# Optimization experiments

Hardware: AMD Instinct MI355X
Metric: run time of the kernel (lower is better)

## Reference

```python
import jax, jax.numpy as jnp
import numpy as np

UNITS = 50

def setup_inputs() -> dict:
    key = jax.random.key(0)
    ks = jax.random.split(key, 6)
    B, T, F = 4096, 128, 64
    scale = 0.1
    return {
        "x": jax.random.normal(ks[0], (B, T, F), dtype=jnp.float32),
        "W": jax.random.normal(ks[1], (F, 3 * UNITS), dtype=jnp.float32) * scale,
        "U": jax.random.normal(ks[2], (UNITS, 3 * UNITS), dtype=jnp.float32) * scale,
        "b": jax.random.normal(ks[3], (2, 3 * UNITS), dtype=jnp.float32) * scale,
        "Wd": jax.random.normal(ks[4], (UNITS, 1), dtype=jnp.float32) * scale,
        "bd": jnp.zeros((1,), dtype=jnp.float32),
    }

def reference(x, W, U, b, Wd, bd):
    # Keras GRU, reset_after=True, activation=relu, recurrent_activation=sigmoid.
    B, T, F = x.shape
    u = UNITS
    # Precompute input projections for all timesteps: [B,T,3u]
    xp = jnp.einsum('btf,fk->btk', x, W) + b[0]
    xp = jnp.moveaxis(xp, 1, 0)  # [T,B,3u]
    bi = b[1]

    def step(h, xt):
        hp = h @ U + bi                     # [B,3u]
        xz, xr, xh = xt[:, :u], xt[:, u:2*u], xt[:, 2*u:]
        hz, hr, hh = hp[:, :u], hp[:, u:2*u], hp[:, 2*u:]
        z = jax.nn.sigmoid(xz + hz)
        r = jax.nn.sigmoid(xr + hr)
        hcand = jax.nn.relu(xh + r * hh)
        h_new = z * h + (1.0 - z) * hcand
        return h_new, None

    h0 = jnp.zeros((B, u), dtype=x.dtype)
    hT, _ = jax.lax.scan(step, h0, xp)
    # Dropout is identity at inference; Dense head:
    return hT @ Wd + bd
```

## Files before the change

### kernel.cpp

```cpp
#include <hip/hip_runtime.h>
#include <math.h>

typedef _Float16 v8h __attribute__((ext_vector_type(8)));
typedef float v4f __attribute__((ext_vector_type(4)));

#define UNITS    50
#define K3       150
#define FDIM     64
#define TSTEPS   128
#define BATCH    4096
#define NB       16
#define H16S     72
#define H32S     52

#if __has_builtin(__builtin_amdgcn_exp2f)
__device__ __forceinline__ float fast_exp2(float x) { return __builtin_amdgcn_exp2f(x); }
#else
__device__ __forceinline__ float fast_exp2(float x) { return exp2f(x); }
#endif
#if __has_builtin(__builtin_amdgcn_rcpf)
__device__ __forceinline__ float fast_rcp(float x) { return __builtin_amdgcn_rcpf(x); }
#else
__device__ __forceinline__ float fast_rcp(float x) { return 1.0f / x; }
#endif

__global__ __launch_bounds__(256, 1)
void gru_4w(const float* __restrict__ x, const float* __restrict__ W,
            const float* __restrict__ U, const float* __restrict__ bv,
            const float* __restrict__ Wd, const float* __restrict__ bd,
            float* __restrict__ out) {
    __shared__ _Float16 hs16[2][NB * H16S];
    __shared__ float    hs32[NB * H32S];

    const int tid  = threadIdx.x;
    const int nt   = tid >> 6;
    const int lane = tid & 63;
    const int n    = lane & 15;
    const int quad = lane >> 4;
    const int b0   = blockIdx.x * NB;
    const int c    = nt * 16 + n;

    for (int i = tid; i < NB * H16S; i += 256) {
        _Float16 v = ((i % H16S) == 50) ? (_Float16)1.f : (_Float16)0.f;
        hs16[0][i] = v;
        hs16[1][i] = v;
    }

    v8h Bz[4], Br[4], Bh[4];
    #pragma unroll
    for (int kt = 0; kt < 4; ++kt) {
        v8h fz, fr, fh;
        #pragma unroll
        for (int j = 0; j < 8; ++j) {
            const int k = kt * 32 + quad * 8 + j;
            float vz = 0.f, vr = 0.f, vh = 0.f;
            if (c < UNITS) {
                if (k < FDIM) {
                    vz = W[k * K3 + c];
                    vr = W[k * K3 + 50 + c];
                    vh = W[k * K3 + 100 + c];
                } else if (k < FDIM + UNITS) {
                    const int ur = k - FDIM;
                    vz = U[ur * K3 + c];
                    vr = U[ur * K3 + 50 + c];
                    vh = U[ur * K3 + 100 + c];
                } else if (k == FDIM + UNITS) {
                    vh = bv[250 + c];
                }
            }
            fz[j] = (_Float16)vz; fr[j] = (_Float16)vr; fh[j] = (_Float16)vh;
        }
        Bz[kt] = fz; Br[kt] = fr; Bh[kt] = fh;
    }

    const float CE = -1.44269504f;
    float bzc = 0.f, brc = 0.f, bx = 0.f;
    if (c < UNITS) {
        bzc = CE * (bv[c]      + bv[150 + c]);
        brc = CE * (bv[50 + c] + bv[200 + c]);
        bx  = bv[100 + c];
    }

    v4f h32 = {0.f, 0.f, 0.f, 0.f};

    const float* xbase = x + ((size_t)(b0 + n) * TSTEPS) * FDIM + quad * 8;
    v4f px0 = *(const v4f*)(xbase + 0);
    v4f px1 = *(const v4f*)(xbase + 4);
    v4f px2 = *(const v4f*)(xbase + 32);
    v4f px3 = *(const v4f*)(xbase + 36);

    __syncthreads();

    for (int t = 0; t < TSTEPS; ++t) {
        const _Float16* hrd = hs16[t & 1];
        _Float16*       hwr = hs16[(t + 1) & 1];

        v8h A0, A1;
        #pragma unroll
        for (int j = 0; j < 4; ++j) {
            A0[j]     = (_Float16)px0[j];
            A0[j + 4] = (_Float16)px1[j];
            A1[j]     = (_Float16)px2[j];
            A1[j + 4] = (_Float16)px3[j];
        }
        v8h A2 = *(const v8h*)(&hrd[n * H16S + quad * 8]);
        v8h A3 = *(const v8h*)(&hrd[n * H16S + 32 + quad * 8]);

        if (t + 1 < TSTEPS) {
            const float* xp = xbase + (size_t)(t + 1) * FDIM;
            px0 = *(const v4f*)(xp + 0);
            px1 = *(const v4f*)(xp + 4);
            px2 = *(const v4f*)(xp + 32);
            px3 = *(const v4f*)(xp + 36);
        }

        const v4f zero4 = {0.f, 0.f, 0.f, 0.f};
        v4f ax = {bx, bx, bx, bx};
        v4f az = __builtin_amdgcn_mfma_f32_16x16x32_f16(A0, Bz[0], zero4, 0, 0, 0);
        az     = __builtin_amdgcn_mfma_f32_16x16x32_f16(A1, Bz[1], az,    0, 0, 0);
        v4f ar = __builtin_amdgcn_mfma_f32_16x16x32_f16(A0, Br[0], zero4, 0, 0, 0);
        ar     = __builtin_amdgcn_mfma_f32_16x16x32_f16(A1, Br[1], ar,    0, 0, 0);
        ax     = __builtin_amdgcn_mfma_f32_16x16x32_f16(A0, Bh[0], ax,    0, 0, 0);
        ax     = __builtin_amdgcn_mfma_f32_16x16x32_f16(A1, Bh[1], ax,    0, 0, 0);
        az     = __builtin_amdgcn_mfma_f32_16x16x32_f16(A2, Bz[2], az,    0, 0, 0);
        az     = __builtin_amdgcn_mfma_f32_16x16x32_f16(A3, Bz[3], az,    0, 0, 0);
        ar     = __builtin_amdgcn_mfma_f32_16x16x32_f16(A2, Br[2], ar,    0, 0, 0);
        ar     = __builtin_amdgcn_mfma_f32_16x16x32_f16(A3, Br[3], ar,    0, 0, 0);
        v4f ah = __builtin_amdgcn_mfma_f32_16x16x32_f16(A2, Bh[2], zero4, 0, 0, 0);
        ah     = __builtin_amdgcn_mfma_f32_16x16x32_f16(A3, Bh[3], ah,    0, 0, 0);

        #pragma unroll
        for (int r = 0; r < 4; ++r) {
            const float ez = fast_exp2(fmaf(az[r], CE, bzc));
            const float er = fast_exp2(fmaf(ar[r], CE, brc));
            const float pz = 1.f + ez;
            const float pr = 1.f + er;
            const float d  = fast_rcp(pz * pr);
            const float zg = d * pr;
            const float rg = d * pz;
            const float hc = fmaxf(fmaf(rg, ah[r], ax[r]), 0.f);
            const float hn = fmaf(zg, h32[r] - hc, hc);
            h32[r] = hn;
            if (c < UNITS)
                hwr[(quad * 4 + r) * H16S + c] = (_Float16)hn;
        }
        __syncthreads();
    }

    if (c < UNITS) {
        #pragma unroll
        for (int r = 0; r < 4; ++r)
            hs32[(quad * 4 + r) * H32S + c] = h32[r];
    }
    __syncthreads();
    if (tid < NB) {
        float acc = bd[0];
        #pragma unroll
        for (int u = 0; u < UNITS; ++u)
            acc = fmaf(hs32[tid * H32S + u], Wd[u], acc);
        out[b0 + tid] = acc;
    }
}

extern "C" void kernel_launch(void* const* d_in, const int* in_sizes, int n_in,
                              void* d_out, int out_size, void* d_ws, size_t ws_size,
                              hipStream_t stream) {
    const float* x    = (const float*)d_in[0];
    const float* W    = (const float*)d_in[1];
    const float* U    = (const float*)d_in[2];
    const float* bv   = (const float*)d_in[3];
    const float* Wd   = (const float*)d_in[4];
    const float* bd   = (const float*)d_in[5];
    float* out = (float*)d_out;

    dim3 grid(BATCH / NB);
    dim3 block(256);
    gru_4w<<<grid, block, 0, stream>>>(x, W, U, bv, Wd, bd, out);
}
```

Before: 272.7 us.

## Use LDS-only barrier, double-buffer x prefetch, split x/h MFMA chains

```diff
diff --git a/kernel.cpp b/kernel.cpp
--- a/kernel.cpp
+++ b/kernel.cpp
@@ -24,11 +24,16 @@
 __device__ __forceinline__ float fast_rcp(float x) { return 1.0f / x; }
 #endif
 
+__device__ __forceinline__ void sync_lds() {
+    asm volatile("s_waitcnt lgkmcnt(0)" ::: "memory");
+    __builtin_amdgcn_s_barrier();
+}
+
 __global__ __launch_bounds__(256, 1)
-void gru_4w(const float* __restrict__ x, const float* __restrict__ W,
-            const float* __restrict__ U, const float* __restrict__ bv,
-            const float* __restrict__ Wd, const float* __restrict__ bd,
-            float* __restrict__ out) {
+void gru_nodrain(const float* __restrict__ x, const float* __restrict__ W,
+                 const float* __restrict__ U, const float* __restrict__ bv,
+                 const float* __restrict__ Wd, const float* __restrict__ bd,
+                 float* __restrict__ out) {
     __shared__ _Float16 hs16[2][NB * H16S];
     __shared__ float    hs32[NB * H32S];
 
@@ -84,67 +89,76 @@
     v4f h32 = {0.f, 0.f, 0.f, 0.f};
 
     const float* xbase = x + ((size_t)(b0 + n) * TSTEPS) * FDIM + quad * 8;
-    v4f px0 = *(const v4f*)(xbase + 0);
-    v4f px1 = *(const v4f*)(xbase + 4);
-    v4f px2 = *(const v4f*)(xbase + 32);
-    v4f px3 = *(const v4f*)(xbase + 36);
+    v4f px[2][4];
+    #pragma unroll
+    for (int s = 0; s < 2; ++s) {
+        const float* xp = xbase + (size_t)s * FDIM;
+        px[s][0] = *(const v4f*)(xp + 0);
+        px[s][1] = *(const v4f*)(xp + 4);
+        px[s][2] = *(const v4f*)(xp + 32);
+        px[s][3] = *(const v4f*)(xp + 36);
+    }
 
     __syncthreads();
 
+    #pragma unroll 2
     for (int t = 0; t < TSTEPS; ++t) {
+        const int pb = t & 1;
         const _Float16* hrd = hs16[t & 1];
         _Float16*       hwr = hs16[(t + 1) & 1];
 
+        v8h A2 = *(const v8h*)(&hrd[n * H16S + quad * 8]);
+        v8h A3 = *(const v8h*)(&hrd[n * H16S + 32 + quad * 8]);
         v8h A0, A1;
         #pragma unroll
         for (int j = 0; j < 4; ++j) {
-            A0[j]     = (_Float16)px0[j];
-            A0[j + 4] = (_Float16)px1[j];
-            A1[j]     = (_Float16)px2[j];
-            A1[j + 4] = (_Float16)px3[j];
+            A0[j]     = (_Float16)px[pb][0][j];
+            A0[j + 4] = (_Float16)px[pb][1][j];
+            A1[j]     = (_Float16)px[pb][2][j];
+            A1[j + 4] = (_Float16)px[pb][3][j];
         }
-        v8h A2 = *(const v8h*)(&hrd[n * H16S + quad * 8]);
-        v8h A3 = *(const v8h*)(&hrd[n * H16S + 32 + quad * 8]);
 
-        if (t + 1 < TSTEPS) {
-            const float* xp = xbase + (size_t)(t + 1) * FDIM;
-            px0 = *(const v4f*)(xp + 0);
-            px1 = *(const v4f*)(xp + 4);
-            px2 = *(const v4f*)(xp + 32);
-            px3 = *(const v4f*)(xp + 36);
+        if (t + 2 < TSTEPS) {
+            const float* xp = xbase + (size_t)(t + 2) * FDIM;
+            px[pb][0] = *(const v4f*)(xp + 0);
+            px[pb][1] = *(const v4f*)(xp + 4);
+            px[pb][2] = *(const v4f*)(xp + 32);
+            px[pb][3] = *(const v4f*)(xp + 36);
         }
 
         const v4f zero4 = {0.f, 0.f, 0.f, 0.f};
-        v4f ax = {bx, bx, bx, bx};
-        v4f az = __builtin_amdgcn_mfma_f32_16x16x32_f16(A0, Bz[0], zero4, 0, 0, 0);
-        az     = __builtin_amdgcn_mfma_f32_16x16x32_f16(A1, Bz[1], az,    0, 0, 0);
-        v4f ar = __builtin_amdgcn_mfma_f32_16x16x32_f16(A0, Br[0], zero4, 0, 0, 0);
-        ar     = __builtin_amdgcn_mfma_f32_16x16x32_f16(A1, Br[1], ar,    0, 0, 0);
-        ax     = __builtin_amdgcn_mfma_f32_16x16x32_f16(A0, Bh[0], ax,    0, 0, 0);
-        ax     = __builtin_amdgcn_mfma_f32_16x16x32_f16(A1, Bh[1], ax,    0, 0, 0);
-        az     = __builtin_amdgcn_mfma_f32_16x16x32_f16(A2, Bz[2], az,    0, 0, 0);
-        az     = __builtin_amdgcn_mfma_f32_16x16x32_f16(A3, Bz[3], az,    0, 0, 0);
-        ar     = __builtin_amdgcn_mfma_f32_16x16x32_f16(A2, Br[2], ar,    0, 0, 0);
-        ar     = __builtin_amdgcn_mfma_f32_16x16x32_f16(A3, Br[3], ar,    0, 0, 0);
-        v4f ah = __builtin_amdgcn_mfma_f32_16x16x32_f16(A2, Bh[2], zero4, 0, 0, 0);
-        ah     = __builtin_amdgcn_mfma_f32_16x16x32_f16(A3, Bh[3], ah,    0, 0, 0);
+        v4f axx = {bx, bx, bx, bx};
+        v4f azx = __builtin_amdgcn_mfma_f32_16x16x32_f16(A0, Bz[0], zero4, 0, 0, 0);
+        azx     = __builtin_amdgcn_mfma_f32_16x16x32_f16(A1, Bz[1], azx,   0, 0, 0);
+        v4f arx = __builtin_amdgcn_mfma_f32_16x16x32_f16(A0, Br[0], zero4, 0, 0, 0);
+        arx     = __builtin_amdgcn_mfma_f32_16x16x32_f16(A1, Br[1], arx,   0, 0, 0);
+        axx     = __builtin_amdgcn_mfma_f32_16x16x32_f16(A0, Bh[0], axx,   0, 0, 0);
+        axx     = __builtin_amdgcn_mfma_f32_16x16x32_f16(A1, Bh[1], axx,   0, 0, 0);
+        v4f azh = __builtin_amdgcn_mfma_f32_16x16x32_f16(A2, Bz[2], zero4, 0, 0, 0);
+        azh     = __builtin_amdgcn_mfma_f32_16x16x32_f16(A3, Bz[3], azh,   0, 0, 0);
+        v4f arh = __builtin_amdgcn_mfma_f32_16x16x32_f16(A2, Br[2], zero4, 0, 0, 0);
+        arh     = __builtin_amdgcn_mfma_f32_16x16x32_f16(A3, Br[3], arh,   0, 0, 0);
+        v4f ahh = __builtin_amdgcn_mfma_f32_16x16x32_f16(A2, Bh[2], zero4, 0, 0, 0);
+        ahh     = __builtin_amdgcn_mfma_f32_16x16x32_f16(A3, Bh[3], ahh,   0, 0, 0);
 
         #pragma unroll
         for (int r = 0; r < 4; ++r) {
-            const float ez = fast_exp2(fmaf(az[r], CE, bzc));
-            const float er = fast_exp2(fmaf(ar[r], CE, brc));
+            const float az = azx[r] + azh[r];
+            const float ar = arx[r] + arh[r];
+            const float ez = fast_exp2(fmaf(az, CE, bzc));
+            const float er = fast_exp2(fmaf(ar, CE, brc));
             const float pz = 1.f + ez;
             const float pr = 1.f + er;
             const float d  = fast_rcp(pz * pr);
             const float zg = d * pr;
             const float rg = d * pz;
-            const float hc = fmaxf(fmaf(rg, ah[r], ax[r]), 0.f);
+            const float hc = fmaxf(fmaf(rg, ahh[r], axx[r]), 0.f);
             const float hn = fmaf(zg, h32[r] - hc, hc);
             h32[r] = hn;
             if (c < UNITS)
                 hwr[(quad * 4 + r) * H16S + c] = (_Float16)hn;
         }
-        __syncthreads();
+        sync_lds();
     }
 
     if (c < UNITS) {
@@ -175,5 +189,5 @@
 
     dim3 grid(BATCH / NB);
     dim3 block(256);
-    gru_4w<<<grid, block, 0, stream>>>(x, W, U, bv, Wd, bd, out);
+    gru_nodrain<<<grid, block, 0, stream>>>(x, W, U, bv, Wd, bd, out);
 }
```

Result: no change. 277.7 us (+1.8%).
